# Kernel tuning notes

Hardware: AMD Instinct MI355X
Metric: run time of the kernel (lower is better)

## Reference

```python
import jax, jax.numpy as jnp
import numpy as np

# LABEL2ID assumed: O=0, B-PERSON=1, I-PERSON=2 (standard tagset ordering)
B_ID = 1
I_ID = 2
SMOOTH = 1e-5
B_WEIGHT = 3.0
I_END_WEIGHT = 2.5
CONTEXT_WEIGHT = 1.5
N_TOKENS = 8388608
NUM_CLASSES = 9


def setup_inputs() -> dict:
    key = jax.random.key(0)
    k1, k2 = jax.random.split(key)
    inputs = jax.random.normal(k1, (N_TOKENS, NUM_CLASSES), dtype=jnp.float32)
    targets = jax.random.randint(k2, (N_TOKENS,), 0, NUM_CLASSES)
    return {"inputs": inputs, "targets": targets}


def _boundary_weights(t):
    # base weight 1; B-PERSON -> b_weight
    w = jnp.ones(t.shape, jnp.float32)
    w = jnp.where(t == B_ID, B_WEIGHT, w)
    # I-PERSON followed by non-I-PERSON -> i_end_weight
    # (torch pads shifted with the last element, so the final I is never flagged here)
    nxt_dup = jnp.concatenate([t[1:], t[-1:]])
    w = jnp.where((t == I_ID) & (nxt_dup != I_ID), I_END_WEIGHT, w)
    # token immediately before a B-PERSON -> context_weight (overwrites prior weights,
    # matching torch's later scatter assignment; index -1 for a leading B is filtered out)
    nxt0 = jnp.concatenate([t[1:], jnp.zeros((1,), t.dtype)])
    w = jnp.where(nxt0 == B_ID, CONTEXT_WEIGHT, w)
    return w


def reference(inputs, targets):
    probs = jax.nn.softmax(inputs, axis=1)                      # [N, C]
    one_hot = jax.nn.one_hot(targets, NUM_CLASSES, dtype=jnp.float32)
    w = _boundary_weights(targets)[:, None]                     # [N, 1]
    intersection = jnp.sum(probs * one_hot * w, axis=0)         # [C]
    denominator = jnp.sum(probs * w, axis=0) + jnp.sum(one_hot * w, axis=0)
    dice_coef = (2.0 * intersection + SMOOTH) / (denominator + SMOOTH)
    return 1.0 - dice_coef.mean()
```

## Files before the change

### kernel.cpp

```cpp
#include <hip/hip_runtime.h>

#define NC 9
#define BLOCK 256
#define TPT 4
#define CHUNK (BLOCK * TPT)
#define GRID 2048


__global__ __launch_bounds__(BLOCK) void dice_partial(
    const float* __restrict__ logits,
    const int*   __restrict__ targets,
    float*       __restrict__ partials,
    int n)
{
    float sWP[NC], sI[NC], sOH[NC];
    #pragma unroll
    for (int c = 0; c < NC; ++c) { sWP[c] = 0.f; sI[c] = 0.f; sOH[c] = 0.f; }

    const int tid = threadIdx.x;
    const int nChunks = (n + CHUNK - 1) / CHUNK;

    for (int chunk = blockIdx.x; chunk < nChunks; chunk += gridDim.x) {
        const int base = chunk * CHUNK + tid * TPT;

        if (base + TPT <= n) {
            const float4* g4 = reinterpret_cast<const float4*>(logits + (size_t)base * NC);
            float f[TPT * NC];
            #pragma unroll
            for (int k = 0; k < 9; ++k) {
                const float4 q = g4[k];
                f[4 * k]     = q.x;
                f[4 * k + 1] = q.y;
                f[4 * k + 2] = q.z;
                f[4 * k + 3] = q.w;
            }
            const int4 t4 = *reinterpret_cast<const int4*>(targets + base);
            int tg[TPT];
            tg[0] = t4.x; tg[1] = t4.y; tg[2] = t4.z; tg[3] = t4.w;
            const int tExtra = (base + TPT < n) ? targets[base + TPT] : 0;
            const bool lastIsGlobalEnd = (base + TPT == n);

            #pragma unroll
            for (int j = 0; j < TPT; ++j) {
                const int  t    = tg[j];
                const bool last = (j == TPT - 1) && lastIsGlobalEnd;
                const int  tn   = (j < TPT - 1) ? tg[j + 1] : tExtra;

                float w = 1.0f;
                if (t == 1) w = 3.0f;
                const int nxt_dup = last ? t : tn;
                if (t == 2 && nxt_dup != 2) w = 2.5f;
                if (!last && tn == 1) w = 1.5f;

                float v[NC];
                #pragma unroll
                for (int c = 0; c < NC; ++c) v[c] = f[j * NC + c];
                float m = v[0];
                #pragma unroll
                for (int c = 1; c < NC; ++c) m = fmaxf(m, v[c]);
                float s = 0.f;
                #pragma unroll
                for (int c = 0; c < NC; ++c) { v[c] = __expf(v[c] - m); s += v[c]; }
                const float inv = __builtin_amdgcn_rcpf(s);

                #pragma unroll
                for (int c = 0; c < NC; ++c) {
                    const float p   = v[c] * inv;
                    const bool  hit = (t == c);
                    sWP[c] += w * p;
                    sI[c]  += hit ? w * p : 0.f;
                    sOH[c] += hit ? w : 0.f;
                }
            }
        } else {
            for (int j = 0; j < TPT; ++j) {
                const int a = base + j;
                if (a >= n) break;
                const int  t    = targets[a];
                const bool last = (a == n - 1);
                const int  tn   = last ? 0 : targets[a + 1];

                float w = 1.0f;
                if (t == 1) w = 3.0f;
                const int nxt_dup = last ? t : tn;
                if (t == 2 && nxt_dup != 2) w = 2.5f;
                if (!last && tn == 1) w = 1.5f;

                float v[NC];
                #pragma unroll
                for (int c = 0; c < NC; ++c) v[c] = logits[(size_t)a * NC + c];
                float m = v[0];
                #pragma unroll
                for (int c = 1; c < NC; ++c) m = fmaxf(m, v[c]);
                float s = 0.f;
                #pragma unroll
                for (int c = 0; c < NC; ++c) { v[c] = __expf(v[c] - m); s += v[c]; }
                const float inv = __builtin_amdgcn_rcpf(s);

                #pragma unroll
                for (int c = 0; c < NC; ++c) {
                    const float p   = v[c] * inv;
                    const bool  hit = (t == c);
                    sWP[c] += w * p;
                    sI[c]  += hit ? w * p : 0.f;
                    sOH[c] += hit ? w : 0.f;
                }
            }
        }
    }

    #pragma unroll
    for (int off = 32; off; off >>= 1) {
        #pragma unroll
        for (int c = 0; c < NC; ++c) {
            sWP[c] += __shfl_down(sWP[c], off);
            sI[c]  += __shfl_down(sI[c], off);
            sOH[c] += __shfl_down(sOH[c], off);
        }
    }

    __shared__ float red[4][32];
    const int lane = tid & 63;
    const int wid  = tid >> 6;
    if (lane == 0) {
        #pragma unroll
        for (int c = 0; c < NC; ++c) {
            red[wid][c]      = sWP[c];
            red[wid][9 + c]  = sI[c];
            red[wid][18 + c] = sOH[c];
        }
    }
    __syncthreads();
    if (tid < 27) {
        partials[blockIdx.x * 32 + tid] =
            red[0][tid] + red[1][tid] + red[2][tid] + red[3][tid];
    }
}

__global__ __launch_bounds__(1024) void dice_reduce(
    const float* __restrict__ partials,
    float*       __restrict__ out,
    int nblocks)
{
    const int c = threadIdx.x & 31;
    const int r = threadIdx.x >> 5;
    float s = 0.f;
    if (c < 27) {
        for (int b = r; b < nblocks; b += 32)
            s += partials[b * 32 + c];
    }
    __shared__ float acc[32][33];
    acc[r][c] = s;
    __syncthreads();
    if (threadIdx.x == 0) {
        float A[27];
        #pragma unroll
        for (int i = 0; i < 27; ++i) {
            float tot = 0.f;
            for (int k = 0; k < 32; ++k) tot += acc[k][i];
            A[i] = tot;
        }
        float dsum = 0.f;
        #pragma unroll
        for (int cc = 0; cc < NC; ++cc) {
            const float inter = A[9 + cc];
            const float den   = A[cc] + A[18 + cc];
            dsum += (2.f * inter + 1e-5f) / (den + 1e-5f);
        }
        out[0] = 1.f - dsum * (1.f / 9.f);
    }
}

extern "C" void kernel_launch(void* const* d_in, const int* in_sizes, int n_in,
                              void* d_out, int out_size, void* d_ws, size_t ws_size,
                              hipStream_t stream)
{
    const float* logits   = (const float*)d_in[0];
    const int*   targets  = (const int*)d_in[1];
    float*       out      = (float*)d_out;
    float*       partials = (float*)d_ws;
    const int n = in_sizes[1];

    const int nChunks = (n + CHUNK - 1) / CHUNK;
    const int grid = nChunks < GRID ? nChunks : GRID;
    dice_partial<<<grid, BLOCK, 0, stream>>>(logits, targets, partials, n);
    dice_reduce<<<1, 1024, 0, stream>>>(partials, out, grid);
}
```

Before: 82.77 us.

## Stage logits through LDS for coalesced loads, double grid, parallelize final reduce

Each wave now loads its 576 float4s of logits with lane-contiguous, fully coalesced global reads, writes them to shared memory, and then reads back each thread's 36 floats. Before, each thread read 9 strided float4s on its own. The grid size doubles to 4096 blocks to put more loads in flight. The final reduce kernel now sums columns with 32 threads instead of a single thread. The LDS round trip adds shared-memory traffic and a 36 KB per-block allocation that may reduce occupancy. Only intra-wave data is shared, so no barrier is needed.

After: 99.28 us. 19.9% more time.

```diff
diff --git a/kernel.cpp b/kernel.cpp
--- a/kernel.cpp
+++ b/kernel.cpp
@@ -4,7 +4,7 @@
 #define BLOCK 256
 #define TPT 4
 #define CHUNK (BLOCK * TPT)
-#define GRID 2048
+#define GRID 4096
 
 
 __global__ __launch_bounds__(BLOCK) void dice_partial(
@@ -13,32 +13,47 @@
     float*       __restrict__ partials,
     int n)
 {
+    __shared__ __align__(16) float4 lds[4 * 576];
+    __shared__ float red[4][32];
+
     float sWP[NC], sI[NC], sOH[NC];
     #pragma unroll
     for (int c = 0; c < NC; ++c) { sWP[c] = 0.f; sI[c] = 0.f; sOH[c] = 0.f; }
 
     const int tid = threadIdx.x;
+    const int w   = tid >> 6;
+    const int l   = tid & 63;
     const int nChunks = (n + CHUNK - 1) / CHUNK;
 
-    for (int chunk = blockIdx.x; chunk < nChunks; chunk += gridDim.x) {
-        const int base = chunk * CHUNK + tid * TPT;
-
-        if (base + TPT <= n) {
-            const float4* g4 = reinterpret_cast<const float4*>(logits + (size_t)base * NC);
+    for (int blk = blockIdx.x; blk < nChunks; blk += gridDim.x) {
+        const int tokBase = blk * CHUNK;
+
+        if (tokBase + CHUNK <= n) {
+            const float4* g4 = reinterpret_cast<const float4*>(logits)
+                             + (size_t)blk * (CHUNK * NC / 4) + w * 576;
+            float4* Lw = lds + w * 576;
+            float4 tmp[9];
+            #pragma unroll
+            for (int k = 0; k < 9; ++k) tmp[k] = g4[k * 64 + l];
+            #pragma unroll
+            for (int k = 0; k < 9; ++k) Lw[k * 64 + l] = tmp[k];
+
             float f[TPT * NC];
             #pragma unroll
             for (int k = 0; k < 9; ++k) {
-                const float4 q = g4[k];
+                const float4 q = Lw[l * 9 + k];
                 f[4 * k]     = q.x;
                 f[4 * k + 1] = q.y;
                 f[4 * k + 2] = q.z;
                 f[4 * k + 3] = q.w;
             }
-            const int4 t4 = *reinterpret_cast<const int4*>(targets + base);
+
+            const int tok0 = tokBase + tid * TPT;
+            const int4 t4  = *reinterpret_cast<const int4*>(targets + tok0);
             int tg[TPT];
             tg[0] = t4.x; tg[1] = t4.y; tg[2] = t4.z; tg[3] = t4.w;
-            const int tExtra = (base + TPT < n) ? targets[base + TPT] : 0;
-            const bool lastIsGlobalEnd = (base + TPT == n);
+            const int  tExtra = (tok0 + TPT < n) ? targets[tok0 + TPT] : 0;
+            const bool lastIsGlobalEnd = (tok0 + TPT == n);
 
             #pragma unroll
             for (int j = 0; j < TPT; ++j) {
@@ -46,11 +61,11 @@
                 const bool last = (j == TPT - 1) && lastIsGlobalEnd;
                 const int  tn   = (j < TPT - 1) ? tg[j + 1] : tExtra;
 
-                float w = 1.0f;
-                if (t == 1) w = 3.0f;
+                float wt = 1.0f;
+                if (t == 1) wt = 3.0f;
                 const int nxt_dup = last ? t : tn;
-                if (t == 2 && nxt_dup != 2) w = 2.5f;
-                if (!last && tn == 1) w = 1.5f;
+                if (t == 2 && nxt_dup != 2) wt = 2.5f;
+                if (!last && tn == 1) wt = 1.5f;
 
                 float v[NC];
                 #pragma unroll
@@ -67,24 +82,24 @@
                 for (int c = 0; c < NC; ++c) {
                     const float p   = v[c] * inv;
                     const bool  hit = (t == c);
-                    sWP[c] += w * p;
-                    sI[c]  += hit ? w * p : 0.f;
-                    sOH[c] += hit ? w : 0.f;
+                    sWP[c] += wt * p;
+                    sI[c]  += hit ? wt * p : 0.f;
+                    sOH[c] += hit ? wt : 0.f;
                 }
             }
         } else {
             for (int j = 0; j < TPT; ++j) {
-                const int a = base + j;
+                const int a = tokBase + tid * TPT + j;
                 if (a >= n) break;
                 const int  t    = targets[a];
                 const bool last = (a == n - 1);
                 const int  tn   = last ? 0 : targets[a + 1];
 
-                float w = 1.0f;
-                if (t == 1) w = 3.0f;
+                float wt = 1.0f;
+                if (t == 1) wt = 3.0f;
                 const int nxt_dup = last ? t : tn;
-                if (t == 2 && nxt_dup != 2) w = 2.5f;
-                if (!last && tn == 1) w = 1.5f;
+                if (t == 2 && nxt_dup != 2) wt = 2.5f;
+                if (!last && tn == 1) wt = 1.5f;
 
                 float v[NC];
                 #pragma unroll
@@ -101,9 +116,9 @@
                 for (int c = 0; c < NC; ++c) {
                     const float p   = v[c] * inv;
                     const bool  hit = (t == c);
-                    sWP[c] += w * p;
-                    sI[c]  += hit ? w * p : 0.f;
-                    sOH[c] += hit ? w : 0.f;
+                    sWP[c] += wt * p;
+                    sI[c]  += hit ? wt * p : 0.f;
+                    sOH[c] += hit ? wt : 0.f;
                 }
             }
         }
@@ -119,15 +134,12 @@
         }
     }
 
-    __shared__ float red[4][32];
-    const int lane = tid & 63;
-    const int wid  = tid >> 6;
-    if (lane == 0) {
+    if (l == 0) {
         #pragma unroll
         for (int c = 0; c < NC; ++c) {
-            red[wid][c]      = sWP[c];
-            red[wid][9 + c]  = sI[c];
-            red[wid][18 + c] = sOH[c];
+            red[w][c]      = sWP[c];
+            red[w][9 + c]  = sI[c];
+            red[w][18 + c] = sOH[c];
         }
     }
     __syncthreads();
@@ -152,14 +164,16 @@
     __shared__ float acc[32][33];
     acc[r][c] = s;
     __syncthreads();
+
+    __shared__ float A[32];
+    if (threadIdx.x < 32) {
+        float tot = 0.f;
+        #pragma unroll
+        for (int k = 0; k < 32; ++k) tot += acc[k][threadIdx.x];
+        A[threadIdx.x] = tot;
+    }
+    __syncthreads();
     if (threadIdx.x == 0) {
-        float A[27];
-        #pragma unroll
-        for (int i = 0; i < 27; ++i) {
-            float tot = 0.f;
-            for (int k = 0; k < 32; ++k) tot += acc[k][i];
-            A[i] = tot;
-        }
         float dsum = 0.f;
         #pragma unroll
         for (int cc = 0; cc < NC; ++cc) {
```
